# Kernel optimization log

Hardware: AMD Instinct MI355X
Metric: run time of the kernel (lower is better)

## Reference

```python
import jax, jax.numpy as jnp
import numpy as np

B, T, IN, H, L, OUT, PRED, FN = 512, 96, 64, 512, 2, 1, 24, 32


def setup_inputs() -> dict:
    key = jax.random.key(0)
    ks = jax.random.split(key, 12)
    sc = 0.02
    n = lambda i, shape: jax.random.normal(ks[i], shape, jnp.float32) * sc
    return {
        "x": jax.random.normal(ks[0], (B, T, IN), jnp.float32),
        "station_id": jax.random.randint(ks[1], (B,), 0, 26, jnp.int32),
        "W_hidden": n(2, (H, IN)), "b_hidden": jnp.zeros((H,), jnp.float32),
        "embed": n(3, (26, H)),
        "W_ih": n(4, (L, 4 * H, H)), "W_hh": n(5, (L, 4 * H, H)),
        "b_ih": jnp.zeros((L, 4 * H), jnp.float32), "b_hh": jnp.zeros((L, 4 * H), jnp.float32),
        "conv_W": n(6, (FN, T - 1)), "conv_b": jnp.zeros((FN,), jnp.float32),
        "W1": n(7, (FN, H)), "b1": jnp.zeros((FN,), jnp.float32),
        "W2": n(8, (H, H + FN)), "b2": jnp.zeros((H,), jnp.float32),
        "W_out": n(9, (T * OUT, H)), "b_out": jnp.zeros((T * OUT,), jnp.float32),
    }


def _lstm(xc, W_ih, W_hh, b_ih, b_hh):
    # xc: [B, T, H]; multi-layer LSTM, PyTorch gate order i,f,g,o
    n_layers = W_ih.shape[0]
    h0 = jnp.zeros((n_layers, xc.shape[0], W_hh.shape[-1]), xc.dtype)

    def step(carry, xt):
        h, c = carry  # [L, B, H]
        inp = xt
        hs, cs = [], []
        for l in range(n_layers):
            g = inp @ W_ih[l].T + h[l] @ W_hh[l].T + b_ih[l] + b_hh[l]
            i, f, gg, o = jnp.split(g, 4, axis=-1)
            cn = jax.nn.sigmoid(f) * c[l] + jax.nn.sigmoid(i) * jnp.tanh(gg)
            hn = jax.nn.sigmoid(o) * jnp.tanh(cn)
            hs.append(hn); cs.append(cn)
            inp = hn
        return (jnp.stack(hs), jnp.stack(cs)), inp  # emit last-layer h

    _, outs = jax.lax.scan(step, (h0, h0), jnp.swapaxes(xc, 0, 1))
    return jnp.swapaxes(outs, 0, 1)  # [B, T, H] last-layer hidden states


def reference(x, station_id, W_hidden, b_hidden, embed, W_ih, W_hh, b_ih, b_hh,
              conv_W, conv_b, W1, b1, W2, b2, W_out, b_out):
    b, t, _ = x.shape
    hdim = W_hidden.shape[0]
    fn = conv_W.shape[0]
    xc = jax.nn.relu(x @ W_hidden.T + b_hidden)
    xc = xc + embed[station_id][:, None, :]
    hs_seq = _lstm(xc, W_ih, W_hh, b_ih, b_hh)          # [B, T, H]
    Hmat = jax.nn.relu(hs_seq[:, :-1, :])                # [B, T-1, H]
    htt = hs_seq[:, -1, :]                               # [B, H]
    # Conv2d(1, FN, (T-1, 1)) over [B,1,T-1,H] == contraction over time
    conv = jax.nn.relu(jnp.einsum('bth,ft->bfh', Hmat, conv_W) + conv_b[None, :, None])
    # original does .view(-1, feat_size, filter_num): raw reshape, not transpose
    feat = conv.reshape(b, hdim, fn)                     # [B, H, FN]
    w = (htt @ W1.T + b1)[:, None, :]                    # [B, 1, FN]
    alpha = jax.nn.sigmoid(jnp.sum(feat * w, axis=2))    # [B, H]
    v = jnp.sum(alpha[:, :, None] * feat, axis=1)        # [B, FN]
    new_ht = jnp.concatenate([htt, v], axis=1) @ W2.T + b2
    ypred = (new_ht @ W_out.T + b_out)[:, -PRED * OUT:]
    return ypred
```

## Files before the change

### kernel.cpp

```cpp
#include <hip/hip_runtime.h>
#include <math.h>

namespace {

constexpr int B = 512, T = 96, IN = 64, H = 512, G4 = 2048;
constexpr int FN = 32, KC = 544, NPRED = 24, TM1 = T - 1;
constexpr int BH = B * H;

typedef __attribute__((ext_vector_type(8))) short s8v;
typedef __attribute__((ext_vector_type(16))) float f16v;

__device__ __forceinline__ float sigf(float x) { return 1.0f / (1.0f + __expf(-x)); }
__device__ __forceinline__ float tanhfast(float x) {
  x = fminf(fmaxf(x, -15.f), 15.f);
  float e = __expf(2.0f * x);
  return (e - 1.0f) / (e + 1.0f);
}
__device__ __forceinline__ unsigned short bf16_rne(float f) {
  unsigned u = __float_as_uint(f);
  u += 0x7fffu + ((u >> 16) & 1u);
  return (unsigned short)(u >> 16);
}
__device__ __forceinline__ void split8(const float4& x, const float4& y, s8v& hi, s8v& lo) {
  float vs[8] = {x.x, x.y, x.z, x.w, y.x, y.y, y.z, y.w};
#pragma unroll
  for (int j = 0; j < 8; ++j) {
    unsigned ub = __float_as_uint(vs[j]);
    hi[j] = (short)(ub >> 16);
    lo[j] = (short)bf16_rne(vs[j] - __uint_as_float(ub & 0xffff0000u));
  }
}

__global__ __launch_bounds__(256) void k_xc(
    const float* __restrict__ x, const int* __restrict__ sid,
    const float* __restrict__ Wh, const float* __restrict__ bh,
    const float* __restrict__ emb, float* __restrict__ planes) {
  constexpr int RB = 8;
  int row0 = blockIdx.x * RB;
  int tid = threadIdx.x;
  __shared__ float sx[RB][IN];
  __shared__ int ssid[RB];
  for (int i = tid; i < RB * IN; i += 256) sx[i / IN][i % IN] = x[(size_t)row0 * IN + i];
  if (tid < RB) ssid[tid] = sid[(row0 + tid) / T];
  __syncthreads();
  for (int h = tid; h < H; h += 256) {
    const float* w = Wh + (size_t)h * IN;
    float b0 = bh[h];
    float acc[RB];
#pragma unroll
    for (int r = 0; r < RB; ++r) acc[r] = b0;
    for (int k = 0; k < IN; ++k) {
      float wv = w[k];
#pragma unroll
      for (int r = 0; r < RB; ++r) acc[r] = fmaf(sx[r][k], wv, acc[r]);
    }
#pragma unroll
    for (int r = 0; r < RB; ++r) {
      int row = row0 + r;
      int bb = row / T, t = row % T;
      float v = fmaxf(acc[r], 0.f) + emb[(size_t)ssid[r] * H + h];
      planes[((size_t)t * B + bb) * H + h] = v;
    }
  }
}

__global__ __launch_bounds__(256) void k_wswz(
    const float* __restrict__ Wih, const float* __restrict__ Whh,
    short* __restrict__ WFhi, short* __restrict__ WFlo) {
  int g = blockIdx.x * 256 + threadIdx.x;
  int lane = g & 63;
  int fi = g >> 6;
  int nt = fi & 3, kt = (fi >> 2) & 63, ng = (fi >> 8) & 15, layer = fi >> 12;
  int row = nt * H + ng * 32 + (lane & 31);
  int kk = kt * 16 + (lane >> 5) * 8;
  const float* src = (kk < H) ? (Wih + ((size_t)layer * G4 + row) * H + kk)
                              : (Whh + ((size_t)layer * G4 + row) * H + (kk - H));
  float4 f0 = *(const float4*)src, f1 = *(const float4*)(src + 4);
  s8v hi, lo;
  split8(f0, f1, hi, lo);
  size_t o = (size_t)fi * 512 + lane * 8;
  *(s8v*)(WFhi + o) = hi;
  *(s8v*)(WFlo + o) = lo;
}

__global__ __launch_bounds__(256, 2) void k_step(
    int tt, float* __restrict__ planes, const short* __restrict__ WFhi,
    const short* __restrict__ WFlo, short* __restrict__ hFhi,
    short* __restrict__ hFlo, const float* __restrict__ bih,
    const float* __restrict__ bhh, float* __restrict__ c0,
    float* __restrict__ c1) {
  int gid = blockIdx.x;
  int layer = gid >> 8;
  if (layer ? (tt == 0) : (tt == T)) return;
  int id = gid & 255;
  int xcd = id & 7, y = id >> 3;
  int ng = xcd * 2 + (y & 1);
  int bg = y >> 1;
  int b0 = bg * 32;
  int step = layer ? (tt - 1) : tt;
  int tid = threadIdx.x, lane = tid & 63, wk = tid >> 6;
  int l31 = lane & 31, lh = lane >> 5;

  __shared__ float comb[4][4][32][32];

  const float* bi = bih + (size_t)layer * G4;
  const float* bh2 = bhh + (size_t)layer * G4;
  float* cbuf = layer ? c1 : c0;

  int rpar = (step - 1) & 1;
  const float* xbase = nullptr;
  const short *abhi = nullptr, *ablo = nullptr;
  if (layer == 0 && wk < 2) {
    xbase = planes + (size_t)step * BH + (size_t)(b0 + l31) * H + wk * 256 + lh * 8;
  } else {
    int src = (layer == 0) ? 0 : ((wk < 2) ? 0 : 1);
    int par = (layer == 0) ? rpar : ((wk < 2) ? (step & 1) : rpar);
    int kk0 = wk * 16 - ((layer == 0 || wk >= 2) ? 32 : 0);
    size_t o = ((((size_t)src * 2 + par) * 32 + kk0) * H + (b0 + l31)) * 16 + lh * 8;
    abhi = hFhi + o;
    ablo = hFlo + o;
  }

  float bias[4];
#pragma unroll
  for (int nt = 0; nt < 4; ++nt) {
    int r = nt * H + ng * 32 + l31;
    bias[nt] = bi[r] + bh2[r];
  }

  const size_t wstep = 4 * 512;
  const size_t wbase0 = ((size_t)(layer * 16 + ng) * 64 + wk * 16) * wstep + (size_t)lane * 8;
  const size_t astep = (size_t)H * 16;

  f16v acc[4];
#pragma unroll
  for (int nt = 0; nt < 4; ++nt)
#pragma unroll
    for (int e = 0; e < 16; ++e) acc[nt][e] = 0.f;

  s8v a0h, a0l, b0h0, b0h1, b0h2, b0h3, b0l0, b0l1, b0l2, b0l3;
  s8v a1h, a1l, b1h0, b1h1, b1h2, b1h3, b1l0, b1l1, b1l2, b1l3;

#define LOADW_(kq, bh0, bh1, bh2, bh3, bl0, bl1, bl2, bl3)          \
  {                                                                 \
    size_t wo = wbase0 + (size_t)(kq) * wstep;                      \
    bh0 = *(const s8v*)(WFhi + wo);                                 \
    bh1 = *(const s8v*)(WFhi + wo + 512);                           \
    bh2 = *(const s8v*)(WFhi + wo + 1024);                          \
    bh3 = *(const s8v*)(WFhi + wo + 1536);                          \
    bl0 = *(const s8v*)(WFlo + wo);                                 \
    bl1 = *(const s8v*)(WFlo + wo + 512);                           \
    bl2 = *(const s8v*)(WFlo + wo + 1024);                          \
    bl3 = *(const s8v*)(WFlo + wo + 1536);                          \
  }
#define LOADA_(kq, ah, al)                                          \
  {                                                                 \
    if (xbase) {                                                    \
      const float* ap = xbase + (kq) * 16;                          \
      float4 f0 = *(const float4*)ap, f1 = *(const float4*)(ap + 4);\
      split8(f0, f1, ah, al);                                       \
    } else {                                                        \
      ah = *(const s8v*)(abhi + (size_t)(kq) * astep);              \
      al = *(const s8v*)(ablo + (size_t)(kq) * astep);              \
    }                                                               \
  }
#define MFMA3_(ah, al, bh0, bh1, bh2, bh3, bl0, bl1, bl2, bl3)                         \
  {                                                                                    \
    acc[0] = __builtin_amdgcn_mfma_f32_32x32x16_bf16(ah, bh0, acc[0], 0, 0, 0);        \
    acc[1] = __builtin_amdgcn_mfma_f32_32x32x16_bf16(ah, bh1, acc[1], 0, 0, 0);        \
    acc[2] = __builtin_amdgcn_mfma_f32_32x32x16_bf16(ah, bh2, acc[2], 0, 0, 0);        \
    acc[3] = __builtin_amdgcn_mfma_f32_32x32x16_bf16(ah, bh3, acc[3], 0, 0, 0);        \
    acc[0] = __builtin_amdgcn_mfma_f32_32x32x16_bf16(ah, bl0, acc[0], 0, 0, 0);        \
    acc[1] = __builtin_amdgcn_mfma_f32_32x32x16_bf16(ah, bl1, acc[1], 0, 0, 0);        \
    acc[2] = __builtin_amdgcn_mfma_f32_32x32x16_bf16(ah, bl2, acc[2], 0, 0, 0);        \
    acc[3] = __builtin_amdgcn_mfma_f32_32x32x16_bf16(ah, bl3, acc[3], 0, 0, 0);        \
    acc[0] = __builtin_amdgcn_mfma_f32_32x32x16_bf16(al, bh0, acc[0], 0, 0, 0);        \
    acc[1] = __builtin_amdgcn_mfma_f32_32x32x16_bf16(al, bh1, acc[1], 0, 0, 0);        \
    acc[2] = __builtin_amdgcn_mfma_f32_32x32x16_bf16(al, bh2, acc[2], 0, 0, 0);        \
    acc[3] = __builtin_amdgcn_mfma_f32_32x32x16_bf16(al, bh3, acc[3], 0, 0, 0);        \
  }

  LOADA_(0, a0h, a0l);
  LOADW_(0, b0h0, b0h1, b0h2, b0h3, b0l0, b0l1, b0l2, b0l3);
#pragma unroll 1
  for (int kp = 0; kp < 8; ++kp) {
    int kq = kp * 2;
    LOADA_(kq + 1, a1h, a1l);
    LOADW_(kq + 1, b1h0, b1h1, b1h2, b1h3, b1l0, b1l1, b1l2, b1l3);
    MFMA3_(a0h, a0l, b0h0, b0h1, b0h2, b0h3, b0l0, b0l1, b0l2, b0l3);
    if (kp < 7) {
      LOADA_(kq + 2, a0h, a0l);
      LOADW_(kq + 2, b0h0, b0h1, b0h2, b0h3, b0l0, b0l1, b0l2, b0l3);
    }
    MFMA3_(a1h, a1l, b1h0, b1h1, b1h2, b1h3, b1l0, b1l1, b1l2, b1l3);
  }
#undef LOADW_
#undef LOADA_
#undef MFMA3_

#pragma unroll
  for (int nt = 0; nt < 4; ++nt)
#pragma unroll
    for (int r = 0; r < 16; ++r) {
      int row = (r & 3) + 8 * (r >> 2) + 4 * lh;
      comb[nt][wk][row][l31] = acc[nt][r];
    }
  __syncthreads();
  if (wk == 0) {
#pragma unroll
    for (int r = 0; r < 16; ++r) {
      int row = (r & 3) + 8 * (r >> 2) + 4 * lh;
      float g[4];
#pragma unroll
      for (int nt = 0; nt < 4; ++nt) {
        float p0 = comb[nt][0][row][l31];
        float p1 = comb[nt][1][row][l31];
        float p2 = comb[nt][2][row][l31];
        float p3 = comb[nt][3][row][l31];
        g[nt] = (p0 + p1) + (p2 + p3) + bias[nt];
      }
      size_t coff = (size_t)(b0 + row) * H + ng * 32 + l31;
      float cp = cbuf[coff];
      float cn = sigf(g[1]) * cp + sigf(g[0]) * tanhfast(g[2]);
      float hn = sigf(g[3]) * tanhfast(cn);
      cbuf[coff] = cn;
      int brow = b0 + row;
      int hcol = ng * 32 + l31;
      size_t o = ((((size_t)layer * 2 + (step & 1)) * 32 + (hcol >> 4)) * H + brow) * 16 + (hcol & 15);
      unsigned ub = __float_as_uint(hn);
      hFhi[o] = (short)(ub >> 16);
      hFlo[o] = (short)bf16_rne(hn - __uint_as_float(ub & 0xffff0000u));
      if (layer) planes[(size_t)step * BH + (size_t)brow * H + hcol] = hn;
    }
  }
}

__global__ __launch_bounds__(256) void k_conv(
    const float* __restrict__ hs, const float* __restrict__ cW,
    const float* __restrict__ cb, float* __restrict__ feat) {
  int b = blockIdx.x >> 2;
  int h0 = (blockIdx.x & 3) * 128;
  int tid = threadIdx.x;
  __shared__ float sW[TM1][FN];
  for (int i = tid; i < TM1 * FN; i += 256) sW[i >> 5][i & 31] = cW[(i & 31) * TM1 + (i >> 5)];
  __syncthreads();
  int hl = tid & 127, fg = (tid >> 7) * 16;
  float acc[16];
#pragma unroll
  for (int j = 0; j < 16; ++j) acc[j] = cb[fg + j];
  const float* hp = hs + (size_t)b * H + h0 + hl;
  for (int t = 0; t < TM1; ++t) {
    float v = fmaxf(hp[(size_t)t * BH], 0.f);
#pragma unroll
    for (int j = 0; j < 16; ++j) acc[j] = fmaf(v, sW[t][fg + j], acc[j]);
  }
#pragma unroll
  for (int j = 0; j < 16; ++j)
    feat[(size_t)b * (FN * H) + (size_t)(fg + j) * H + h0 + hl] = fmaxf(acc[j], 0.f);
}

__global__ __launch_bounds__(256) void k_attn(
    const float* __restrict__ hs, const float* __restrict__ feat,
    const float* __restrict__ W1, const float* __restrict__ b1,
    const float* __restrict__ W2, const float* __restrict__ b2,
    const float* __restrict__ Wout, const float* __restrict__ bout,
    float* __restrict__ out) {
  int b = blockIdx.x, tid = threadIdx.x;
  __shared__ float sh[H], sa[H], snew[H], sw[FN], sv[FN], red[256];
  const float* htt = hs + (size_t)(T - 1) * BH + (size_t)b * H;
  for (int i = tid; i < H; i += 256) sh[i] = htt[i];
  __syncthreads();
  {
    int f = tid >> 3, sl = tid & 7;
    const float* w1 = W1 + (size_t)f * H;
    float p = 0.f;
    for (int k = sl * 64; k < sl * 64 + 64; ++k) p = fmaf(sh[k], w1[k], p);
    p += __shfl_xor(p, 1); p += __shfl_xor(p, 2); p += __shfl_xor(p, 4);
    if (sl == 0) sw[f] = p + b1[f];
  }
  __syncthreads();
  const float* fb = feat + (size_t)b * (FN * H);
  for (int i = tid; i < H; i += 256) {
    const float* fr = fb + (size_t)i * FN;
    float p = 0.f;
#pragma unroll
    for (int j = 0; j < FN; ++j) p = fmaf(fr[j], sw[j], p);
    sa[i] = sigf(p);
  }
  __syncthreads();
  {
    int j = tid & 31, isl = tid >> 5;
    float p = 0.f;
    for (int i = isl * 64; i < isl * 64 + 64; ++i) p = fmaf(sa[i], fb[(size_t)i * FN + j], p);
    red[tid] = p;
  }
  __syncthreads();
  if (tid < 128) red[tid] += red[tid + 128];
  __syncthreads();
  if (tid < 64) red[tid] += red[tid + 64];
  __syncthreads();
  if (tid < 32) sv[tid] = red[tid] + red[tid + 32];
  __syncthreads();
  for (int h = tid; h < H; h += 256) {
    const float* w2 = W2 + (size_t)h * KC;
    float p = b2[h];
    for (int k = 0; k < H; ++k) p = fmaf(sh[k], w2[k], p);
#pragma unroll
    for (int j = 0; j < FN; ++j) p = fmaf(sv[j], w2[H + j], p);
    snew[h] = p;
  }
  __syncthreads();
  if (tid < NPRED * 8) {
    int p = tid >> 3, sl = tid & 7;
    const float* wo = Wout + (size_t)(T - NPRED + p) * H;
    float sacc = 0.f;
    for (int k = sl * 64; k < sl * 64 + 64; ++k) sacc = fmaf(snew[k], wo[k], sacc);
    sacc += __shfl_xor(sacc, 1); sacc += __shfl_xor(sacc, 2); sacc += __shfl_xor(sacc, 4);
    if (sl == 0) out[(size_t)b * NPRED + p] = sacc + bout[T - NPRED + p];
  }
}

}

extern "C" void kernel_launch(void* const* d_in, const int* in_sizes, int n_in,
                              void* d_out, int out_size, void* d_ws, size_t ws_size,
                              hipStream_t stream) {
  const float* x    = (const float*)d_in[0];
  const int*   sid  = (const int*)d_in[1];
  const float* Wh   = (const float*)d_in[2];
  const float* bh   = (const float*)d_in[3];
  const float* emb  = (const float*)d_in[4];
  const float* Wih  = (const float*)d_in[5];
  const float* Whh  = (const float*)d_in[6];
  const float* bih  = (const float*)d_in[7];
  const float* bhh  = (const float*)d_in[8];
  const float* cW   = (const float*)d_in[9];
  const float* cb   = (const float*)d_in[10];
  const float* W1   = (const float*)d_in[11];
  const float* b1   = (const float*)d_in[12];
  const float* W2   = (const float*)d_in[13];
  const float* b2   = (const float*)d_in[14];
  const float* Wout = (const float*)d_in[15];
  const float* bout = (const float*)d_in[16];
  float* out = (float*)d_out;

  constexpr size_t HFE = (size_t)2 * 2 * 32 * H * 16;
  float* planes = (float*)d_ws;
  short* WFhi = (short*)(planes + (size_t)T * BH);
  short* WFlo = WFhi + (size_t)8192 * 512;
  short* hFhi = WFlo + (size_t)8192 * 512;
  short* hFlo = hFhi + HFE;
  float* cst = (float*)(hFlo + HFE);
  float* c0 = cst;
  float* c1 = cst + BH;
  float* feat = c1 + BH;
  size_t need = (size_t)T * BH * 4 + (size_t)8192 * 512 * 2 * 2 + HFE * 2 * 2 +
                2 * (size_t)BH * 4 + (size_t)B * FN * H * 4;
  if (ws_size < need) return;

  hipMemsetAsync(hFhi, 0, HFE * 2 * 2 + 2 * (size_t)BH * 4, stream);
  k_xc<<<(B * T) / 8, 256, 0, stream>>>(x, sid, Wh, bh, emb, planes);
  k_wswz<<<2048, 256, 0, stream>>>(Wih, Whh, WFhi, WFlo);

  for (int tt = 0; tt <= T; ++tt)
    k_step<<<512, 256, 0, stream>>>(tt, planes, WFhi, WFlo, hFhi, hFlo, bih, bhh, c0, c1);

  k_conv<<<B * 4, 256, 0, stream>>>(planes, cW, cb, feat);
  k_attn<<<B, 256, 0, stream>>>(planes, feat, W1, b1, W2, b2, Wout, bout, out);
}
```

Baseline: 2.614 ms.

## Deepen LSTM step prefetch, remap block ids, spread epilogue, vectorize side kernels

The LSTM step kernel now keeps three k-slices of weights and activations in flight instead of two, and remaps block ids so layer and batch groups spread differently across XCDs. The gate epilogue is split over all four waves instead of only wave 0. The input projection kernel stages the weight matrix transposed in shared memory, and the head kernel uses float4 loads for its dot products. The deeper prefetch raises register pressure in k_step, which could cut occupancy below the two-blocks-per-CU launch bound.

```diff
diff --git a/kernel.cpp b/kernel.cpp
--- a/kernel.cpp
+++ b/kernel.cpp
@@ -38,21 +38,38 @@
   constexpr int RB = 8;
   int row0 = blockIdx.x * RB;
   int tid = threadIdx.x;
-  __shared__ float sx[RB][IN];
+  __shared__ float sW[IN][257];
   __shared__ int ssid[RB];
-  for (int i = tid; i < RB * IN; i += 256) sx[i / IN][i % IN] = x[(size_t)row0 * IN + i];
   if (tid < RB) ssid[tid] = sid[(row0 + tid) / T];
-  __syncthreads();
-  for (int h = tid; h < H; h += 256) {
-    const float* w = Wh + (size_t)h * IN;
+  for (int hc = 0; hc < 2; ++hc) {
+    __syncthreads();
+    for (int i = tid; i < 256 * IN; i += 256) {
+      int h = i >> 6, k = i & 63;
+      sW[k][h] = Wh[(size_t)(hc * 256 + h) * IN + k];
+    }
+    __syncthreads();
+    int h = hc * 256 + tid;
     float b0 = bh[h];
     float acc[RB];
 #pragma unroll
     for (int r = 0; r < RB; ++r) acc[r] = b0;
-    for (int k = 0; k < IN; ++k) {
-      float wv = w[k];
-#pragma unroll
-      for (int r = 0; r < RB; ++r) acc[r] = fmaf(sx[r][k], wv, acc[r]);
+#pragma unroll 4
+    for (int kc = 0; kc < IN / 4; ++kc) {
+      float4 xv[RB];
+#pragma unroll
+      for (int r = 0; r < RB; ++r)
+        xv[r] = *(const float4*)(x + (size_t)(row0 + r) * IN + kc * 4);
+      float w0 = sW[kc * 4 + 0][tid];
+      float w1 = sW[kc * 4 + 1][tid];
+      float w2 = sW[kc * 4 + 2][tid];
+      float w3 = sW[kc * 4 + 3][tid];
+#pragma unroll
+      for (int r = 0; r < RB; ++r) {
+        acc[r] = fmaf(xv[r].x, w0, acc[r]);
+        acc[r] = fmaf(xv[r].y, w1, acc[r]);
+        acc[r] = fmaf(xv[r].z, w2, acc[r]);
+        acc[r] = fmaf(xv[r].w, w3, acc[r]);
+      }
     }
 #pragma unroll
     for (int r = 0; r < RB; ++r) {
@@ -90,12 +107,13 @@
     const float* __restrict__ bhh, float* __restrict__ c0,
     float* __restrict__ c1) {
   int gid = blockIdx.x;
-  int layer = gid >> 8;
+  int xcd = gid & 7;
+  int u = gid >> 3;
+  int v = u & 31, aa = u >> 5;
+  int layer = v >> 4;
   if (layer ? (tt == 0) : (tt == T)) return;
-  int id = gid & 255;
-  int xcd = id & 7, y = id >> 3;
-  int ng = xcd * 2 + (y & 1);
-  int bg = y >> 1;
+  int ng = xcd * 2 + ((v >> 3) & 1);
+  int bg = (v & 7) | (aa << 3);
   int b0 = bg * 32;
   int step = layer ? (tt - 1) : tt;
   int tid = threadIdx.x, lane = tid & 63, wk = tid >> 6;
@@ -140,6 +158,7 @@
 
   s8v a0h, a0l, b0h0, b0h1, b0h2, b0h3, b0l0, b0l1, b0l2, b0l3;
   s8v a1h, a1l, b1h0, b1h1, b1h2, b1h3, b1l0, b1l1, b1l2, b1l3;
+  s8v a2h, a2l, b2h0, b2h1, b2h2, b2h3, b2l0, b2l1, b2l2, b2l3;
 
 #define LOADW_(kq, bh0, bh1, bh2, bh3, bl0, bl1, bl2, bl3)          \
   {                                                                 \
@@ -182,18 +201,28 @@
 
   LOADA_(0, a0h, a0l);
   LOADW_(0, b0h0, b0h1, b0h2, b0h3, b0l0, b0l1, b0l2, b0l3);
+  LOADA_(1, a1h, a1l);
+  LOADW_(1, b1h0, b1h1, b1h2, b1h3, b1l0, b1l1, b1l2, b1l3);
+  LOADA_(2, a2h, a2l);
+  LOADW_(2, b2h0, b2h1, b2h2, b2h3, b2l0, b2l1, b2l2, b2l3);
 #pragma unroll 1
-  for (int kp = 0; kp < 8; ++kp) {
-    int kq = kp * 2;
-    LOADA_(kq + 1, a1h, a1l);
-    LOADW_(kq + 1, b1h0, b1h1, b1h2, b1h3, b1l0, b1l1, b1l2, b1l3);
+  for (int kp = 0; kp < 5; ++kp) {
+    int kq = kp * 3;
     MFMA3_(a0h, a0l, b0h0, b0h1, b0h2, b0h3, b0l0, b0l1, b0l2, b0l3);
-    if (kp < 7) {
-      LOADA_(kq + 2, a0h, a0l);
-      LOADW_(kq + 2, b0h0, b0h1, b0h2, b0h3, b0l0, b0l1, b0l2, b0l3);
-    }
+    LOADA_(kq + 3, a0h, a0l);
+    LOADW_(kq + 3, b0h0, b0h1, b0h2, b0h3, b0l0, b0l1, b0l2, b0l3);
     MFMA3_(a1h, a1l, b1h0, b1h1, b1h2, b1h3, b1l0, b1l1, b1l2, b1l3);
-  }
+    if (kp < 4) {
+      LOADA_(kq + 4, a1h, a1l);
+      LOADW_(kq + 4, b1h0, b1h1, b1h2, b1h3, b1l0, b1l1, b1l2, b1l3);
+    }
+    MFMA3_(a2h, a2l, b2h0, b2h1, b2h2, b2h3, b2l0, b2l1, b2l2, b2l3);
+    if (kp < 4) {
+      LOADA_(kq + 5, a2h, a2l);
+      LOADW_(kq + 5, b2h0, b2h1, b2h2, b2h3, b2l0, b2l1, b2l2, b2l3);
+    }
+  }
+  MFMA3_(a0h, a0l, b0h0, b0h1, b0h2, b0h3, b0l0, b0l1, b0l2, b0l3);
 #undef LOADW_
 #undef LOADA_
 #undef MFMA3_
@@ -206,32 +235,31 @@
       comb[nt][wk][row][l31] = acc[nt][r];
     }
   __syncthreads();
-  if (wk == 0) {
-#pragma unroll
-    for (int r = 0; r < 16; ++r) {
-      int row = (r & 3) + 8 * (r >> 2) + 4 * lh;
-      float g[4];
-#pragma unroll
-      for (int nt = 0; nt < 4; ++nt) {
-        float p0 = comb[nt][0][row][l31];
-        float p1 = comb[nt][1][row][l31];
-        float p2 = comb[nt][2][row][l31];
-        float p3 = comb[nt][3][row][l31];
-        g[nt] = (p0 + p1) + (p2 + p3) + bias[nt];
-      }
-      size_t coff = (size_t)(b0 + row) * H + ng * 32 + l31;
-      float cp = cbuf[coff];
-      float cn = sigf(g[1]) * cp + sigf(g[0]) * tanhfast(g[2]);
-      float hn = sigf(g[3]) * tanhfast(cn);
-      cbuf[coff] = cn;
-      int brow = b0 + row;
-      int hcol = ng * 32 + l31;
-      size_t o = ((((size_t)layer * 2 + (step & 1)) * 32 + (hcol >> 4)) * H + brow) * 16 + (hcol & 15);
-      unsigned ub = __float_as_uint(hn);
-      hFhi[o] = (short)(ub >> 16);
-      hFlo[o] = (short)bf16_rne(hn - __uint_as_float(ub & 0xffff0000u));
-      if (layer) planes[(size_t)step * BH + (size_t)brow * H + hcol] = hn;
-    }
+#pragma unroll
+  for (int rr = 0; rr < 4; ++rr) {
+    int r = wk * 4 + rr;
+    int row = (r & 3) + 8 * (r >> 2) + 4 * lh;
+    float g[4];
+#pragma unroll
+    for (int nt = 0; nt < 4; ++nt) {
+      float p0 = comb[nt][0][row][l31];
+      float p1 = comb[nt][1][row][l31];
+      float p2 = comb[nt][2][row][l31];
+      float p3 = comb[nt][3][row][l31];
+      g[nt] = (p0 + p1) + (p2 + p3) + bias[nt];
+    }
+    size_t coff = (size_t)(b0 + row) * H + ng * 32 + l31;
+    float cp = cbuf[coff];
+    float cn = sigf(g[1]) * cp + sigf(g[0]) * tanhfast(g[2]);
+    float hn = sigf(g[3]) * tanhfast(cn);
+    cbuf[coff] = cn;
+    int brow = b0 + row;
+    int hcol = ng * 32 + l31;
+    size_t o = ((((size_t)layer * 2 + (step & 1)) * 32 + (hcol >> 4)) * H + brow) * 16 + (hcol & 15);
+    unsigned ub = __float_as_uint(hn);
+    hFhi[o] = (short)(ub >> 16);
+    hFlo[o] = (short)bf16_rne(hn - __uint_as_float(ub & 0xffff0000u));
+    if (layer) planes[(size_t)step * BH + (size_t)brow * H + hcol] = hn;
   }
 }
 
@@ -284,7 +312,13 @@
     const float* fr = fb + (size_t)i * FN;
     float p = 0.f;
 #pragma unroll
-    for (int j = 0; j < FN; ++j) p = fmaf(fr[j], sw[j], p);
+    for (int j = 0; j < FN; j += 4) {
+      float4 fv = *(const float4*)(fr + j);
+      p = fmaf(fv.x, sw[j], p);
+      p = fmaf(fv.y, sw[j + 1], p);
+      p = fmaf(fv.z, sw[j + 2], p);
+      p = fmaf(fv.w, sw[j + 3], p);
+    }
     sa[i] = sigf(p);
   }
   __syncthreads();
@@ -304,9 +338,23 @@
   for (int h = tid; h < H; h += 256) {
     const float* w2 = W2 + (size_t)h * KC;
     float p = b2[h];
-    for (int k = 0; k < H; ++k) p = fmaf(sh[k], w2[k], p);
-#pragma unroll
-    for (int j = 0; j < FN; ++j) p = fmaf(sv[j], w2[H + j], p);
+#pragma unroll 4
+    for (int k = 0; k < H; k += 4) {
+      float4 wv = *(const float4*)(w2 + k);
+      float4 shv = *(const float4*)(sh + k);
+      p = fmaf(shv.x, wv.x, p);
+      p = fmaf(shv.y, wv.y, p);
+      p = fmaf(shv.z, wv.z, p);
+      p = fmaf(shv.w, wv.w, p);
+    }
+#pragma unroll
+    for (int j = 0; j < FN; j += 4) {
+      float4 wv = *(const float4*)(w2 + H + j);
+      p = fmaf(sv[j], wv.x, p);
+      p = fmaf(sv[j + 1], wv.y, p);
+      p = fmaf(sv[j + 2], wv.z, p);
+      p = fmaf(sv[j + 3], wv.w, p);
+    }
     snew[h] = p;
   }
   __syncthreads();
```

After: 2.417 ms. 1.08x faster.
